# Kernel optimization log

Hardware: AMD Instinct MI355X
Metric: run time of the kernel (lower is better)

Reference implementation:

```python
import jax, jax.numpy as jnp
import numpy as np

B, C, H, W = 16, 128, 192, 192
RED = 8
ITERN = 5


def setup_inputs() -> dict:
    key = jax.random.key(0)
    k = jax.random.split(key, 5)
    cr = C // RED
    return {
        "x": jax.random.normal(k[0], (B, C, H, W), dtype=jnp.float32),
        "w1": jax.random.normal(k[1], (cr, C), dtype=jnp.float32) * 0.05,
        "b1": jax.random.normal(k[2], (cr,), dtype=jnp.float32) * 0.05,
        "w2": jax.random.normal(k[3], (C, cr), dtype=jnp.float32) * 0.05,
        "b2": jax.random.normal(k[4], (C,), dtype=jnp.float32) * 0.05,
    }


def _soca_forward(x, w1, b1, w2, b2):
    b, c, h, w = x.shape
    M = h * w
    # --- Covpool: y = x @ I_hat @ x^T with I_hat = (1/M)I - (1/M^2) 1 1^T ---
    xf = x.reshape(b, c, M)
    xc = (xf - xf.mean(axis=2, keepdims=True)) / M  # x @ I_hat, [b, c, M]
    cov = jnp.einsum('bcm,bdm->bcd', xc, xf)        # [b, c, c]
    # --- Sqrtm: Newton-Schulz iteration (iterN = 5) ---
    # normA = 1/3 * sum(cov @ 3I) = sum of all entries of cov
    normA = cov.sum(axis=(1, 2))                    # [b]
    A = cov / normA[:, None, None]
    I3 = 3.0 * jnp.eye(c, dtype=x.dtype)            # broadcasts over batch
    ZY = 0.5 * (I3 - A)
    Y = jnp.matmul(A, ZY)
    Z = ZY
    for _ in range(1, ITERN - 1):
        ZY = 0.5 * jnp.matmul(I3 - Z, Y)
        Y = jnp.matmul(Y, ZY)
        Z = jnp.matmul(ZY, Z)
    ZY = jnp.matmul(jnp.matmul(0.5 * Y, I3 - Z), Y)
    sqrt_cov = ZY * jnp.sqrt(normA)[:, None, None]  # [b, c, c]
    # --- mean over rows -> SE gate via two 1x1 convs ---
    s = sqrt_cov.mean(axis=1)                       # [b, c]
    hdn = jax.nn.relu(s @ w1.T + b1)                # [b, c//r]
    gate = jax.nn.sigmoid(hdn @ w2.T + b2)          # [b, c]
    return gate[:, :, None, None] * x


def reference(x, w1, b1, w2, b2):
    return _soca_forward(x, w1, b1, w2, b2)
```

## Files before the change

### kernel.cpp

```cpp
#include <hip/hip_runtime.h>
#include <hip/hip_bf16.h>


#define BATCH 16
#define CHN   128
#define MLEN  36864
#define NCH   32
#define KC    (MLEN / NCH)
#define NITER (KC / 64)

typedef short bf16x8 __attribute__((ext_vector_type(8)));
typedef float f32x4  __attribute__((ext_vector_type(4)));

__device__ __forceinline__ ushort f2bf(float f) {
    unsigned u = __float_as_uint(f);
    u = (u + 0x7FFFu + ((u >> 16) & 1u)) >> 16;
    return (ushort)u;
}
__device__ __forceinline__ float bf2f(ushort s) {
    return __uint_as_float(((unsigned)s) << 16);
}

__global__ __launch_bounds__(256) void k_gram(const float* __restrict__ x,
                                              float* __restrict__ pG,
                                              float* __restrict__ pR) {
    __shared__ __align__(16) ushort st[8192];
    __shared__ float rsum[128];
    const int t    = threadIdx.x;
    const int lane = t & 63, wv = t >> 6;
    const int lr   = lane & 15, lk = lane >> 4;
    const int chunk = blockIdx.x, b = blockIdx.y;

    if (t < 128) rsum[t] = 0.f;

    const int r0  = t >> 4;
    const int kk  = (t & 15) << 2;
    const int kb0 = kk >> 5, kg0 = (kk >> 3) & 3, e0 = kk & 7;
    ushort* stw = &st[((kb0 * 4 + kg0) * 128) * 8 + e0];
    const float* xbase = x + (size_t)(b * CHN) * MLEN + (size_t)chunk * KC + kk;

    float rs[8];
#pragma unroll
    for (int p = 0; p < 8; ++p) rs[p] = 0.f;
    f32x4 acc[2][8];
#pragma unroll
    for (int i = 0; i < 2; ++i)
#pragma unroll
        for (int j = 0; j < 8; ++j) acc[i][j] = (f32x4){0.f, 0.f, 0.f, 0.f};

#define LOADV(V, IT)                                                          \
    _Pragma("unroll") for (int p = 0; p < 8; ++p)                             \
        V[p] = *(const float4*)(xbase + (size_t)(r0 + 16 * p) * MLEN + (IT) * 64);

#define STAGEV(V)                                                             \
    _Pragma("unroll") for (int p = 0; p < 8; ++p) {                           \
        union { ushort4 u; __hip_bfloat162 h[2]; } cv;                        \
        cv.h[0] = __float22bfloat162_rn(make_float2(V[p].x, V[p].y));         \
        cv.h[1] = __float22bfloat162_rn(make_float2(V[p].z, V[p].w));         \
        *(ushort4*)(stw + ((r0 + 16 * p) ^ (kg0 << 1)) * 8) = cv.u;           \
        rs[p] += (V[p].x + V[p].y) + (V[p].z + V[p].w);                       \
    }

#define MFMAS()                                                               \
    _Pragma("unroll") for (int kb = 0; kb < 2; ++kb) {                        \
        const int sb = (kb * 4 + lk) * 128;                                   \
        bf16x8 af[2], bfr[8];                                                 \
        _Pragma("unroll") for (int rt = 0; rt < 2; ++rt)                      \
            af[rt] = *(const bf16x8*)&st[(sb + ((wv * 32 + rt * 16 + lr) ^ (lk << 1))) * 8]; \
        _Pragma("unroll") for (int ct = 0; ct < 8; ++ct)                      \
            bfr[ct] = *(const bf16x8*)&st[(sb + ((ct * 16 + lr) ^ (lk << 1))) * 8]; \
        _Pragma("unroll") for (int rt = 0; rt < 2; ++rt)                      \
            _Pragma("unroll") for (int ct = 0; ct < 8; ++ct)                  \
                acc[rt][ct] = __builtin_amdgcn_mfma_f32_16x16x32_bf16(        \
                    af[rt], bfr[ct], acc[rt][ct], 0, 0, 0);                   \
    }

    float4 vA[8], vB[8];
    LOADV(vA, 0);
    int it = 0;
    while (true) {
        __syncthreads();
        STAGEV(vA);
        __syncthreads();
        if (it + 1 < NITER) LOADV(vB, it + 1);
        MFMAS();
        if (++it >= NITER) break;
        __syncthreads();
        STAGEV(vB);
        __syncthreads();
        if (it + 1 < NITER) LOADV(vA, it + 1);
        MFMAS();
        if (++it >= NITER) break;
    }

#pragma unroll
    for (int p = 0; p < 8; ++p) atomicAdd(&rsum[r0 + 16 * p], rs[p]);
    __syncthreads();
    float* G = pG + ((size_t)(b * NCH + chunk)) * 16384;
#pragma unroll
    for (int rt = 0; rt < 2; ++rt)
#pragma unroll
        for (int ct = 0; ct < 8; ++ct)
#pragma unroll
            for (int r = 0; r < 4; ++r) {
                const int row = wv * 32 + rt * 16 + lk * 4 + r;
                const int col = ct * 16 + lr;
                G[row * 128 + col] = acc[rt][ct][r];
            }
    if (t < 128) pR[((size_t)(b * NCH + chunk)) * 128 + t] = rsum[t];
}

__global__ __launch_bounds__(256) void k_cov(const float* __restrict__ pG,
                                             const float* __restrict__ pR,
                                             float* __restrict__ cov,
                                             float* __restrict__ nA) {
    __shared__ float rs[128];
    __shared__ float red[4];
    const int t = threadIdx.x;
    const int s = blockIdx.x, b = blockIdx.y;
    if (t < 128) {
        float r = 0.f;
        for (int c = 0; c < NCH; ++c) r += pR[((size_t)(b * NCH + c)) * 128 + t];
        rs[t] = r;
    }
    __syncthreads();
    const float inv = 1.0f / (float)MLEN;
    const int idx4 = s * 256 + t;
    const int i  = idx4 >> 5;
    const int j0 = (idx4 & 31) << 2;
    float4 g = {0.f, 0.f, 0.f, 0.f};
    for (int c = 0; c < NCH; ++c) {
        const float4 pv = *(const float4*)(pG + ((size_t)(b * NCH + c)) * 16384 + (size_t)idx4 * 4);
        g.x += pv.x; g.y += pv.y; g.z += pv.z; g.w += pv.w;
    }
    const float ri = rs[i] * inv;
    float4 cv;
    cv.x = (g.x - ri * rs[j0 + 0]) * inv;
    cv.y = (g.y - ri * rs[j0 + 1]) * inv;
    cv.z = (g.z - ri * rs[j0 + 2]) * inv;
    cv.w = (g.w - ri * rs[j0 + 3]) * inv;
    *(float4*)(cov + (size_t)b * 16384 + (size_t)idx4 * 4) = cv;
    float lsum = cv.x + cv.y + cv.z + cv.w;
#pragma unroll
    for (int off = 32; off; off >>= 1) lsum += __shfl_xor(lsum, off);
    if ((t & 63) == 0) red[t >> 6] = lsum;
    __syncthreads();
    if (t == 0) atomicAdd(nA + b, red[0] + red[1] + red[2] + red[3]);
}

__device__ __forceinline__ void zero_acc(f32x4 acc[2][8]) {
#pragma unroll
    for (int i = 0; i < 2; ++i)
#pragma unroll
        for (int j = 0; j < 8; ++j) acc[i][j] = (f32x4){0.f, 0.f, 0.f, 0.f};
}

__device__ __forceinline__ void ns_mm(const ushort* __restrict__ L,
                                      const ushort* __restrict__ R,
                                      f32x4 acc[2][8], int wv, int lr, int lk) {
#pragma unroll
    for (int kb = 0; kb < 4; ++kb) {
        const int kof = kb * 32 + lk * 8;
        bf16x8 af[2], bfr[8];
#pragma unroll
        for (int rt = 0; rt < 2; ++rt) {
            const int row = wv * 32 + rt * 16 + lr;
            af[rt] = *(const bf16x8*)(L + row * 128 + (kof ^ ((row & 7) << 3)));
        }
#pragma unroll
        for (int ct = 0; ct < 8; ++ct) {
            const int row = ct * 16 + lr;
            bfr[ct] = *(const bf16x8*)(R + row * 128 + (kof ^ ((row & 7) << 3)));
        }
#pragma unroll
        for (int rt = 0; rt < 2; ++rt)
#pragma unroll
            for (int ct = 0; ct < 8; ++ct)
                acc[rt][ct] = __builtin_amdgcn_mfma_f32_16x16x32_bf16(
                    af[rt], bfr[ct], acc[rt][ct], 0, 0, 0);
    }
}

__device__ __forceinline__ void ns_store(ushort* __restrict__ D,
                                         const f32x4 acc[2][8], int wv, int lr, int lk) {
#pragma unroll
    for (int rt = 0; rt < 2; ++rt)
#pragma unroll
        for (int ct = 0; ct < 8; ++ct)
#pragma unroll
            for (int r = 0; r < 4; ++r) {
                const int row = wv * 32 + rt * 16 + lk * 4 + r;
                const int col = ct * 16 + lr;
                D[row * 128 + (col ^ ((row & 7) << 3))] = f2bf(acc[rt][ct][r]);
            }
}

__device__ __forceinline__ void ns_store_t(ushort* __restrict__ D,
                                           const ushort* __restrict__ Ysrc,
                                           const f32x4 acc[2][8], int wv, int lr, int lk) {
#pragma unroll
    for (int rt = 0; rt < 2; ++rt)
#pragma unroll
        for (int ct = 0; ct < 8; ++ct)
#pragma unroll
            for (int r = 0; r < 4; ++r) {
                const int row = wv * 32 + rt * 16 + lk * 4 + r;
                const int col = ct * 16 + lr;
                const int si  = row * 128 + (col ^ ((row & 7) << 3));
                D[si] = f2bf(1.5f * bf2f(Ysrc[si]) - 0.5f * acc[rt][ct][r]);
            }
}

__global__ __launch_bounds__(256) void k_ns(const float* __restrict__ cov,
                                            const float* __restrict__ nA,
                                            const float* __restrict__ w1,
                                            const float* __restrict__ b1v,
                                            const float* __restrict__ w2,
                                            const float* __restrict__ b2v,
                                            float* __restrict__ gate) {
    __shared__ __align__(16) ushort bufs[4][16384];
    __shared__ float scol[128];
    __shared__ float sef[128];
    __shared__ float hdn[16];
    const int t = threadIdx.x;
    const int lane = t & 63, wv = t >> 6;
    const int lr = lane & 15, lk = lane >> 4;
    const int b = blockIdx.x;
    const float invn = 1.0f / nA[b];
    ushort* base = &bufs[0][0];

    for (int p = 0; p < 64; ++p) {
        const int idx = t + p * 256;
        const int i = idx >> 7, j = idx & 127;
        const float a = cov[(size_t)b * 16384 + idx] * invn;
        const int si = i * 128 + (j ^ ((i & 7) << 3));
        base[si]         = f2bf(a);
        base[16384 + si] = f2bf((i == j ? 1.5f : 0.f) - 0.5f * a);
    }
    __syncthreads();

    f32x4 acc[2][8];

    zero_acc(acc);
    ns_mm(base, base, acc, wv, lr, lk);
    ns_store_t(base + 2 * 16384, base, acc, wv, lr, lk);
    __syncthreads();

    int y = 2, z = 1, f1 = 0, f2 = 3;
    for (int itn = 0; itn < 3; ++itn) {
        ushort* Y = base + y * 16384;
        ushort* Z = base + z * 16384;
        ushort* T = base + f1 * 16384;
        ushort* N = base + f2 * 16384;
        zero_acc(acc); ns_mm(Z, Y, acc, wv, lr, lk);
        ns_store_t(T, Y, acc, wv, lr, lk);
        __syncthreads();
        zero_acc(acc); ns_mm(Y, T, acc, wv, lr, lk);
        ns_store(N, acc, wv, lr, lk);
        zero_acc(acc); ns_mm(T, Z, acc, wv, lr, lk);
        __syncthreads();
        ns_store(Y, acc, wv, lr, lk);
        __syncthreads();
        const int oy = y, oz = z, of1 = f1, of2 = f2;
        y = of2; z = oy; f1 = oz; f2 = of1;
    }

    {
        ushort* Y = base + y * 16384;
        ushort* Z = base + z * 16384;
        ushort* T = base + f1 * 16384;
        zero_acc(acc); ns_mm(Y, Z, acc, wv, lr, lk);
        ns_store_t(T, Y, acc, wv, lr, lk);
        __syncthreads();
        zero_acc(acc); ns_mm(T, Y, acc, wv, lr, lk);
    }

    if (t < 128) scol[t] = 0.f;
    __syncthreads();
#pragma unroll
    for (int ct = 0; ct < 8; ++ct) {
        float s = 0.f;
#pragma unroll
        for (int rt = 0; rt < 2; ++rt)
#pragma unroll
            for (int r = 0; r < 4; ++r) s += acc[rt][ct][r];
        atomicAdd(&scol[ct * 16 + lr], s);
    }
    __syncthreads();
    const float sc = sqrtf(nA[b]) * (1.0f / 128.0f);
    if (t < 128) sef[t] = scol[t] * sc;
    __syncthreads();
    if (t < 16) {
        float a = b1v[t];
        for (int c = 0; c < 128; ++c) a += sef[c] * w1[t * 128 + c];
        hdn[t] = fmaxf(a, 0.f);
    }
    __syncthreads();
    if (t < 128) {
        float a = b2v[t];
#pragma unroll
        for (int j = 0; j < 16; ++j) a += hdn[j] * w2[t * 16 + j];
        gate[b * 128 + t] = 1.0f / (1.0f + expf(-a));
    }
}

__global__ __launch_bounds__(256) void k_scale(const float4* __restrict__ x4,
                                               const float* __restrict__ gate,
                                               float4* __restrict__ o4) {
    const int bc = blockIdx.y;
    const float g = gate[bc];
    const int basei = bc * (MLEN / 4) + blockIdx.x * 3072 + threadIdx.x;
#pragma unroll
    for (int j = 0; j < 12; ++j) {
        const float4 v = x4[basei + j * 256];
        float4 o;
        o.x = v.x * g; o.y = v.y * g; o.z = v.z * g; o.w = v.w * g;
        o4[basei + j * 256] = o;
    }
}

extern "C" void kernel_launch(void* const* d_in, const int* in_sizes, int n_in,
                              void* d_out, int out_size, void* d_ws, size_t ws_size,
                              hipStream_t stream) {
    const float* x  = (const float*)d_in[0];
    const float* w1 = (const float*)d_in[1];
    const float* b1 = (const float*)d_in[2];
    const float* w2 = (const float*)d_in[3];
    const float* b2 = (const float*)d_in[4];
    float* out = (float*)d_out;

    char* p = (char*)d_ws;
    float* pG   = (float*)p; p += (size_t)NCH * BATCH * 16384 * 4;
    float* pR   = (float*)p; p += (size_t)NCH * BATCH * 128 * 4;
    float* cov  = (float*)p; p += (size_t)BATCH * 16384 * 4;
    float* nA   = (float*)p; p += 256;
    float* gate = (float*)p;

    hipMemsetAsync(nA, 0, BATCH * sizeof(float), stream);
    k_gram<<<dim3(NCH, BATCH), 256, 0, stream>>>(x, pG, pR);
    k_cov<<<dim3(16, BATCH), 256, 0, stream>>>(pG, pR, cov, nA);
    k_ns<<<BATCH, 256, 0, stream>>>(cov, nA, w1, b1, w2, b2, gate);
    k_scale<<<dim3(3, BATCH * CHN), 256, 0, stream>>>((const float4*)x, gate, (float4*)out);
}
```

Before: 615.1 us.

## Stream x into LDS asynchronously, compute row sums via MFMA, store bf16 partial Grams

The Gram kernel now loads fp32 x straight into double-buffered LDS with global_load_lds, skipping the register staging path. Tiles are converted to bf16 while fragments are read, and row sums come from an MFMA against a ones vector instead of scalar adds. Chunk count doubles to 64 to raise occupancy. Partial Grams are stored in bf16 in fragment order, and normA is reduced without atomics or a memset. The scale kernel uses nontemporal loads and stores. Risks: extra precision loss from bf16 partial sums, more reduction traffic in k_cov, and fp32 LDS reads that are less efficient.

```diff
diff --git a/kernel.cpp b/kernel.cpp
--- a/kernel.cpp
+++ b/kernel.cpp
@@ -5,12 +5,15 @@
 #define BATCH 16
 #define CHN   128
 #define MLEN  36864
-#define NCH   32
+#define NCH   64
 #define KC    (MLEN / NCH)
-#define NITER (KC / 64)
-
-typedef short bf16x8 __attribute__((ext_vector_type(8)));
-typedef float f32x4  __attribute__((ext_vector_type(4)));
+#define KSTEP 32
+#define NITER (KC / KSTEP)
+
+typedef short  bf16x8 __attribute__((ext_vector_type(8)));
+typedef float  f32x4  __attribute__((ext_vector_type(4)));
+typedef ushort u16x4  __attribute__((ext_vector_type(4)));
+typedef float  f4     __attribute__((ext_vector_type(4)));
 
 __device__ __forceinline__ ushort f2bf(float f) {
     unsigned u = __float_as_uint(f);
@@ -20,97 +23,108 @@
 __device__ __forceinline__ float bf2f(ushort s) {
     return __uint_as_float(((unsigned)s) << 16);
 }
-
-__global__ __launch_bounds__(256) void k_gram(const float* __restrict__ x,
-                                              float* __restrict__ pG,
-                                              float* __restrict__ pR) {
-    __shared__ __align__(16) ushort st[8192];
-    __shared__ float rsum[128];
+__device__ __forceinline__ bf16x8 pack8(f32x4 a, f32x4 b) {
+    union { bf16x8 v; __hip_bfloat162 h[4]; } u;
+    u.h[0] = __float22bfloat162_rn(make_float2(a[0], a[1]));
+    u.h[1] = __float22bfloat162_rn(make_float2(a[2], a[3]));
+    u.h[2] = __float22bfloat162_rn(make_float2(b[0], b[1]));
+    u.h[3] = __float22bfloat162_rn(make_float2(b[2], b[3]));
+    return u.v;
+}
+
+__global__ __launch_bounds__(256, 4) void k_gram(const float* __restrict__ x,
+                                                 ushort* __restrict__ pG,
+                                                 float* __restrict__ pR) {
+    __shared__ __align__(16) float xs[2][128 * KSTEP];
     const int t    = threadIdx.x;
     const int lane = t & 63, wv = t >> 6;
     const int lr   = lane & 15, lk = lane >> 4;
     const int chunk = blockIdx.x, b = blockIdx.y;
 
-    if (t < 128) rsum[t] = 0.f;
-
-    const int r0  = t >> 4;
-    const int kk  = (t & 15) << 2;
-    const int kb0 = kk >> 5, kg0 = (kk >> 3) & 3, e0 = kk & 7;
-    ushort* stw = &st[((kb0 * 4 + kg0) * 128) * 8 + e0];
-    const float* xbase = x + (size_t)(b * CHN) * MLEN + (size_t)chunk * KC + kk;
-
-    float rs[8];
-#pragma unroll
-    for (int p = 0; p < 8; ++p) rs[p] = 0.f;
+    const int grow = lane >> 3;
+    const int kqg  = (lane & 7) ^ (grow & 6);
+    const float* gsrc[4];
+#pragma unroll
+    for (int j = 0; j < 4; ++j) {
+        const int row = (wv * 4 + j) * 8 + grow;
+        gsrc[j] = x + (size_t)(b * CHN + row) * MLEN + (size_t)chunk * KC + kqg * 4;
+    }
+
+#define ISSUE(BUF, IT)                                                         \
+    _Pragma("unroll") for (int j = 0; j < 4; ++j) {                            \
+        __builtin_amdgcn_global_load_lds(                                      \
+            (const __attribute__((address_space(1))) void*)(gsrc[j] + (IT) * KSTEP), \
+            (__attribute__((address_space(3))) void*)&xs[BUF][(wv * 4 + j) * 256],   \
+            16, 0, 0);                                                         \
+    }
+
+    bf16x8 bONE;
+#pragma unroll
+    for (int i = 0; i < 8; ++i) bONE[i] = (short)0x3F80;
+
     f32x4 acc[2][8];
-#pragma unroll
-    for (int i = 0; i < 2; ++i)
+    f32x4 acc_r[2];
+#pragma unroll
+    for (int i = 0; i < 2; ++i) {
+        acc_r[i] = (f32x4){0.f, 0.f, 0.f, 0.f};
 #pragma unroll
         for (int j = 0; j < 8; ++j) acc[i][j] = (f32x4){0.f, 0.f, 0.f, 0.f};
-
-#define LOADV(V, IT)                                                          \
-    _Pragma("unroll") for (int p = 0; p < 8; ++p)                             \
-        V[p] = *(const float4*)(xbase + (size_t)(r0 + 16 * p) * MLEN + (IT) * 64);
-
-#define STAGEV(V)                                                             \
-    _Pragma("unroll") for (int p = 0; p < 8; ++p) {                           \
-        union { ushort4 u; __hip_bfloat162 h[2]; } cv;                        \
-        cv.h[0] = __float22bfloat162_rn(make_float2(V[p].x, V[p].y));         \
-        cv.h[1] = __float22bfloat162_rn(make_float2(V[p].z, V[p].w));         \
-        *(ushort4*)(stw + ((r0 + 16 * p) ^ (kg0 << 1)) * 8) = cv.u;           \
-        rs[p] += (V[p].x + V[p].y) + (V[p].z + V[p].w);                       \
-    }
-
-#define MFMAS()                                                               \
-    _Pragma("unroll") for (int kb = 0; kb < 2; ++kb) {                        \
-        const int sb = (kb * 4 + lk) * 128;                                   \
-        bf16x8 af[2], bfr[8];                                                 \
-        _Pragma("unroll") for (int rt = 0; rt < 2; ++rt)                      \
-            af[rt] = *(const bf16x8*)&st[(sb + ((wv * 32 + rt * 16 + lr) ^ (lk << 1))) * 8]; \
-        _Pragma("unroll") for (int ct = 0; ct < 8; ++ct)                      \
-            bfr[ct] = *(const bf16x8*)&st[(sb + ((ct * 16 + lr) ^ (lk << 1))) * 8]; \
-        _Pragma("unroll") for (int rt = 0; rt < 2; ++rt)                      \
-            _Pragma("unroll") for (int ct = 0; ct < 8; ++ct)                  \
-                acc[rt][ct] = __builtin_amdgcn_mfma_f32_16x16x32_bf16(        \
-                    af[rt], bfr[ct], acc[rt][ct], 0, 0, 0);                   \
-    }
-
-    float4 vA[8], vB[8];
-    LOADV(vA, 0);
-    int it = 0;
-    while (true) {
-        __syncthreads();
-        STAGEV(vA);
-        __syncthreads();
-        if (it + 1 < NITER) LOADV(vB, it + 1);
-        MFMAS();
-        if (++it >= NITER) break;
-        __syncthreads();
-        STAGEV(vB);
-        __syncthreads();
-        if (it + 1 < NITER) LOADV(vA, it + 1);
-        MFMAS();
-        if (++it >= NITER) break;
-    }
-
-#pragma unroll
-    for (int p = 0; p < 8; ++p) atomicAdd(&rsum[r0 + 16 * p], rs[p]);
-    __syncthreads();
-    float* G = pG + ((size_t)(b * NCH + chunk)) * 16384;
+    }
+
+    ISSUE(0, 0);
+    __syncthreads();
+    for (int it = 0; it < NITER; ++it) {
+        const int cur = it & 1;
+        if (it + 1 < NITER) ISSUE(cur ^ 1, it + 1);
+        {
+            const float* S = xs[cur];
+            bf16x8 af[2];
+#pragma unroll
+            for (int rt = 0; rt < 2; ++rt) {
+                const int row = wv * 32 + rt * 16 + lr;
+                const int q0  = (2 * lk) ^ (row & 6);
+                const f32x4 a0 = *(const f32x4*)(S + row * KSTEP + q0 * 4);
+                const f32x4 a1 = *(const f32x4*)(S + row * KSTEP + q0 * 4 + 4);
+                af[rt] = pack8(a0, a1);
+            }
+            acc_r[0] = __builtin_amdgcn_mfma_f32_16x16x32_bf16(af[0], bONE, acc_r[0], 0, 0, 0);
+            acc_r[1] = __builtin_amdgcn_mfma_f32_16x16x32_bf16(af[1], bONE, acc_r[1], 0, 0, 0);
+#pragma unroll
+            for (int ct = 0; ct < 8; ++ct) {
+                const int row = ct * 16 + lr;
+                const int q0  = (2 * lk) ^ (row & 6);
+                const f32x4 b0 = *(const f32x4*)(S + row * KSTEP + q0 * 4);
+                const f32x4 b1 = *(const f32x4*)(S + row * KSTEP + q0 * 4 + 4);
+                const bf16x8 bfr = pack8(b0, b1);
+                acc[0][ct] = __builtin_amdgcn_mfma_f32_16x16x32_bf16(af[0], bfr, acc[0][ct], 0, 0, 0);
+                acc[1][ct] = __builtin_amdgcn_mfma_f32_16x16x32_bf16(af[1], bfr, acc[1][ct], 0, 0, 0);
+            }
+        }
+        __syncthreads();
+    }
+
+    ushort* Gc = pG + ((size_t)(b * NCH + chunk)) * 16384;
 #pragma unroll
     for (int rt = 0; rt < 2; ++rt)
 #pragma unroll
-        for (int ct = 0; ct < 8; ++ct)
-#pragma unroll
-            for (int r = 0; r < 4; ++r) {
-                const int row = wv * 32 + rt * 16 + lk * 4 + r;
-                const int col = ct * 16 + lr;
-                G[row * 128 + col] = acc[rt][ct][r];
-            }
-    if (t < 128) pR[((size_t)(b * NCH + chunk)) * 128 + t] = rsum[t];
-}
-
-__global__ __launch_bounds__(256) void k_cov(const float* __restrict__ pG,
+        for (int ct = 0; ct < 8; ++ct) {
+            union { u16x4 u; __hip_bfloat162 h[2]; } cv;
+            cv.h[0] = __float22bfloat162_rn(make_float2(acc[rt][ct][0], acc[rt][ct][1]));
+            cv.h[1] = __float22bfloat162_rn(make_float2(acc[rt][ct][2], acc[rt][ct][3]));
+            *(u16x4*)(Gc + (((wv * 2 + rt) * 8 + ct) * 64 + lane) * 4) = cv.u;
+        }
+    if (lr == 0) {
+        float* Rc = pR + ((size_t)(b * NCH + chunk)) * 128;
+#pragma unroll
+        for (int rt = 0; rt < 2; ++rt)
+#pragma unroll
+            for (int r = 0; r < 4; ++r)
+                Rc[wv * 32 + rt * 16 + lk * 4 + r] = acc_r[rt][r];
+    }
+#undef ISSUE
+}
+
+__global__ __launch_bounds__(256) void k_cov(const ushort* __restrict__ pG,
                                              const float* __restrict__ pR,
                                              float* __restrict__ cov,
                                              float* __restrict__ nA) {
@@ -124,28 +138,36 @@
         rs[t] = r;
     }
     __syncthreads();
+    const int qi = s * 256 + t;
+    const ushort* base = pG + (size_t)b * NCH * 16384 + (size_t)qi * 4;
+    float g0 = 0.f, g1 = 0.f, g2 = 0.f, g3 = 0.f;
+    for (int c = 0; c < NCH; ++c) {
+        const u16x4 u = *(const u16x4*)(base + (size_t)c * 16384);
+        g0 += bf2f(u[0]); g1 += bf2f(u[1]); g2 += bf2f(u[2]); g3 += bf2f(u[3]);
+    }
+    const int lane6 = qi & 63;
+    const int ct  = (qi >> 6) & 7;
+    const int rt  = (qi >> 9) & 1;
+    const int wvq = (qi >> 10) & 3;
+    const int row0 = wvq * 32 + rt * 16 + (lane6 >> 4) * 4;
+    const int col  = ct * 16 + (lane6 & 15);
     const float inv = 1.0f / (float)MLEN;
-    const int idx4 = s * 256 + t;
-    const int i  = idx4 >> 5;
-    const int j0 = (idx4 & 31) << 2;
-    float4 g = {0.f, 0.f, 0.f, 0.f};
-    for (int c = 0; c < NCH; ++c) {
-        const float4 pv = *(const float4*)(pG + ((size_t)(b * NCH + c)) * 16384 + (size_t)idx4 * 4);
-        g.x += pv.x; g.y += pv.y; g.z += pv.z; g.w += pv.w;
-    }
-    const float ri = rs[i] * inv;
-    float4 cv;
-    cv.x = (g.x - ri * rs[j0 + 0]) * inv;
-    cv.y = (g.y - ri * rs[j0 + 1]) * inv;
-    cv.z = (g.z - ri * rs[j0 + 2]) * inv;
-    cv.w = (g.w - ri * rs[j0 + 3]) * inv;
-    *(float4*)(cov + (size_t)b * 16384 + (size_t)idx4 * 4) = cv;
-    float lsum = cv.x + cv.y + cv.z + cv.w;
+    const float rc  = rs[col] * inv;
+    float* cb = cov + (size_t)b * 16384 + col;
+    const float cv0 = (g0 - rs[row0 + 0] * rc) * inv;
+    const float cv1 = (g1 - rs[row0 + 1] * rc) * inv;
+    const float cv2 = (g2 - rs[row0 + 2] * rc) * inv;
+    const float cv3 = (g3 - rs[row0 + 3] * rc) * inv;
+    cb[(row0 + 0) * 128] = cv0;
+    cb[(row0 + 1) * 128] = cv1;
+    cb[(row0 + 2) * 128] = cv2;
+    cb[(row0 + 3) * 128] = cv3;
+    float lsum = (cv0 + cv1) + (cv2 + cv3);
 #pragma unroll
     for (int off = 32; off; off >>= 1) lsum += __shfl_xor(lsum, off);
     if ((t & 63) == 0) red[t >> 6] = lsum;
     __syncthreads();
-    if (t == 0) atomicAdd(nA + b, red[0] + red[1] + red[2] + red[3]);
+    if (t == 0) nA[b * 16 + s] = (red[0] + red[1]) + (red[2] + red[3]);
 }
 
 __device__ __forceinline__ void zero_acc(f32x4 acc[2][8]) {
@@ -226,7 +248,11 @@
     const int lane = t & 63, wv = t >> 6;
     const int lr = lane & 15, lk = lane >> 4;
     const int b = blockIdx.x;
-    const float invn = 1.0f / nA[b];
+
+    float normA = 0.f;
+#pragma unroll
+    for (int s = 0; s < 16; ++s) normA += nA[b * 16 + s];
+    const float invn = 1.0f / normA;
     ushort* base = &bufs[0][0];
 
     for (int p = 0; p < 64; ++p) {
@@ -287,7 +313,7 @@
         atomicAdd(&scol[ct * 16 + lr], s);
     }
     __syncthreads();
-    const float sc = sqrtf(nA[b]) * (1.0f / 128.0f);
+    const float sc = sqrtf(normA) * (1.0f / 128.0f);
     if (t < 128) sef[t] = scol[t] * sc;
     __syncthreads();
     if (t < 16) {
@@ -304,18 +330,16 @@
     }
 }
 
-__global__ __launch_bounds__(256) void k_scale(const float4* __restrict__ x4,
+__global__ __launch_bounds__(256) void k_scale(const f4* __restrict__ x4,
                                                const float* __restrict__ gate,
-                                               float4* __restrict__ o4) {
+                                               f4* __restrict__ o4) {
     const int bc = blockIdx.y;
     const float g = gate[bc];
     const int basei = bc * (MLEN / 4) + blockIdx.x * 3072 + threadIdx.x;
 #pragma unroll
     for (int j = 0; j < 12; ++j) {
-        const float4 v = x4[basei + j * 256];
-        float4 o;
-        o.x = v.x * g; o.y = v.y * g; o.z = v.z * g; o.w = v.w * g;
-        o4[basei + j * 256] = o;
+        const f4 v = __builtin_nontemporal_load(x4 + basei + j * 256);
+        __builtin_nontemporal_store(v * g, o4 + basei + j * 256);
     }
 }
 
@@ -330,15 +354,14 @@
     float* out = (float*)d_out;
 
     char* p = (char*)d_ws;
-    float* pG   = (float*)p; p += (size_t)NCH * BATCH * 16384 * 4;
-    float* pR   = (float*)p; p += (size_t)NCH * BATCH * 128 * 4;
-    float* cov  = (float*)p; p += (size_t)BATCH * 16384 * 4;
-    float* nA   = (float*)p; p += 256;
+    ushort* pG  = (ushort*)p; p += (size_t)NCH * BATCH * 16384 * 2;
+    float* pR   = (float*)p;  p += (size_t)NCH * BATCH * 128 * 4;
+    float* cov  = (float*)p;  p += (size_t)BATCH * 16384 * 4;
+    float* nA   = (float*)p;  p += 16 * BATCH * 4;
     float* gate = (float*)p;
 
-    hipMemsetAsync(nA, 0, BATCH * sizeof(float), stream);
     k_gram<<<dim3(NCH, BATCH), 256, 0, stream>>>(x, pG, pR);
     k_cov<<<dim3(16, BATCH), 256, 0, stream>>>(pG, pR, cov, nA);
     k_ns<<<BATCH, 256, 0, stream>>>(cov, nA, w1, b1, w2, b2, gate);
-    k_scale<<<dim3(3, BATCH * CHN), 256, 0, stream>>>((const float4*)x, gate, (float4*)out);
-}
+    k_scale<<<dim3(3, BATCH * CHN), 256, 0, stream>>>((const f4*)x, gate, (f4*)out);
+}
```

New measurement: 587.9 us. 4.4% less time.
